# Performance work log

Hardware: AMD Instinct MI355X
Metric: run time of the kernel (lower is better)

## Reference

```python
import jax, jax.numpy as jnp
import numpy as np

N_NODES = 100000
N_EDGES = 1200000
D = 64          # node_feat_size
G_FEAT = 128    # graph_feat_size
N_GRAPHS = 256
N_TASKS = 1


def setup_inputs() -> dict:
    key = jax.random.key(0)
    ks = jax.random.split(key, 12)
    node_feats = jax.random.normal(ks[0], (N_NODES, D), dtype=jnp.float32)
    edge_feats = jax.random.normal(ks[1], (N_EDGES, 8), dtype=jnp.float32)
    src = jax.random.randint(ks[2], (N_EDGES,), 0, N_NODES, dtype=jnp.int64 if jax.config.read('jax_enable_x64') else jnp.int32)
    dst = jax.random.randint(ks[3], (N_EDGES,), 0, N_NODES, dtype=src.dtype)
    graph_ids = jnp.sort(jax.random.randint(ks[4], (N_NODES,), 0, N_GRAPHS, dtype=src.dtype))
    s = 1.0 / np.sqrt(D)
    W_gcn = jax.random.uniform(ks[5], (D, D), minval=-s, maxval=s, dtype=jnp.float32)
    b_gcn = jnp.zeros((D,), jnp.float32)
    W_res = jax.random.uniform(ks[6], (D, D), minval=-s, maxval=s, dtype=jnp.float32)
    b_res = jnp.zeros((D,), jnp.float32)
    W_in = jax.random.uniform(ks[7], (D, D), minval=-s, maxval=s, dtype=jnp.float32)
    b_in = jnp.zeros((D,), jnp.float32)
    W_out = jax.random.uniform(ks[8], (D, G_FEAT), minval=-s, maxval=s, dtype=jnp.float32)
    b_out = jnp.zeros((G_FEAT,), jnp.float32)
    sp = 1.0 / np.sqrt(G_FEAT)
    W_pred = jax.random.uniform(ks[9], (G_FEAT, N_TASKS), minval=-sp, maxval=sp, dtype=jnp.float32)
    b_pred = jnp.zeros((N_TASKS,), jnp.float32)
    return dict(node_feats=node_feats, edge_feats=edge_feats, src=src, dst=dst,
                graph_ids=graph_ids, W_gcn=W_gcn, b_gcn=b_gcn, W_res=W_res, b_res=b_res,
                W_in=W_in, b_in=b_in, W_out=W_out, b_out=b_out, W_pred=W_pred, b_pred=b_pred)


def reference(node_feats, edge_feats, src, dst, graph_ids,
              W_gcn, b_gcn, W_res, b_res, W_in, b_in, W_out, b_out, W_pred, b_pred):
    # --- GCNLayer (GraphConv norm='none', activation=relu, residual=True) ---
    # message passing: copy src features, sum at dst (no normalization)
    agg = jax.ops.segment_sum(node_feats[src], dst, num_segments=N_NODES)  # [N, D]
    h = jax.nn.relu(agg @ W_gcn + b_gcn)                                   # graph_conv output
    h = h + jax.nn.relu(node_feats @ W_res + b_res)                        # residual branch
    # --- MLPNodeReadout (mode='sum') ---
    h = jax.nn.relu(h @ W_in + b_in)      # [N, D]
    h = h @ W_out + b_out                 # [N, G_FEAT]
    g_feats = jax.ops.segment_sum(h, graph_ids, num_segments=N_GRAPHS)  # [G, G_FEAT]
    # --- predict ---
    out = (g_feats @ W_pred + b_pred).reshape(-1)  # [G * n_tasks]
    return out
```

## Files before the change

### kernel.cpp

```cpp
#include <hip/hip_runtime.h>

typedef __attribute__((ext_vector_type(8))) __bf16 bf16x8;
typedef __attribute__((ext_vector_type(4))) float f32x4;

union Frag { unsigned short u[8]; bf16x8 b; };

__device__ __forceinline__ unsigned short rne_bf16(float x) {
    unsigned int u = __float_as_uint(x);
    return (unsigned short)((u + 0x7fffu + ((u >> 16) & 1u)) >> 16);
}
__device__ __forceinline__ float bf16_to_f(unsigned short h) {
    return __uint_as_float(((unsigned int)h) << 16);
}

#define MFMA16 __builtin_amdgcn_mfma_f32_16x16x32_bf16
#define SBSH 10
#define SBN 1024
#define SBCAP 13056
#define BINCHUNK 4096
#define NWFRAG (3 * 2 * 2 * 4 * 64 * 8)

__global__ __launch_bounds__(256) void prepbinA_kernel(
    const float* __restrict__ nf, const int* __restrict__ src,
    const int* __restrict__ dst,
    const float* __restrict__ Wg, const float* __restrict__ Wr,
    const float* __restrict__ Wi, const float* __restrict__ Wo,
    const float* __restrict__ bo, const float* __restrict__ Wp,
    const float* __restrict__ bp,
    unsigned short* __restrict__ nfb, unsigned short* __restrict__ wfrag,
    float* __restrict__ wfold, float* __restrict__ c0, float* __restrict__ out,
    int* __restrict__ gcursor, int* __restrict__ binned,
    int nBin, int nE, int nbS, int out_size, int nNodes) {
    __shared__ int lhist[128], lbase[128], lofs[128];
    __shared__ int wtot;
    __shared__ int sortedV[BINCHUNK];
    __shared__ int sortedA[BINCHUNK];
    const int t = threadIdx.x;
    if ((int)blockIdx.x < nBin) {
        const int e0 = blockIdx.x * BINCHUNK;
        const int e1 = min(e0 + BINCHUNK, nE);
        const int cnt = e1 - e0;
        if (t < 128) lhist[t] = 0;
        __syncthreads();
        int myr[16];
        #pragma unroll
        for (int u = 0; u < 16; ++u) {
            int e = e0 + t + u * 256;
            if (e < e1) myr[u] = atomicAdd(&lhist[dst[e] >> SBSH], 1);
        }
        __syncthreads();
        int x = 0;
        if (t < 128) {
            x = lhist[t];
            #pragma unroll
            for (int s = 1; s < 64; s <<= 1) {
                int v = __shfl_up(x, s, 64);
                if ((t & 63) >= s) x += v;
            }
            if (t == 63) wtot = x;
        }
        __syncthreads();
        if (t < 128) {
            lofs[t] = x + ((t >= 64) ? wtot : 0);
            if (t < nbS) {
                int c = lhist[t];
                lbase[t] = c ? atomicAdd(&gcursor[t], c) : 0;
            }
        }
        __syncthreads();
        #pragma unroll
        for (int u = 0; u < 16; ++u) {
            int e = e0 + t + u * 256;
            if (e < e1) {
                int d = dst[e];
                int sb = d >> SBSH;
                int r = myr[u];
                int p = (lofs[sb] - lhist[sb]) + r;
                sortedV[p] = (src[e] << SBSH) | (d & (SBN - 1));
                int gp = lbase[sb] + r;
                sortedA[p] = (gp < SBCAP) ? (sb * SBCAP + gp) : -1;
            }
        }
        __syncthreads();
        for (int i = t; i < cnt; i += 256) {
            int ga = sortedA[i];
            if (ga >= 0) binned[ga] = sortedV[i];
        }
        return;
    }
    const int tp = ((int)blockIdx.x - nBin) * 256 + t;
    const int nth = ((int)gridDim.x - nBin) * 256;
    const float4* nf4 = (const float4*)nf;
    ushort4* nfb4 = (ushort4*)nfb;
    const int nQ = nNodes * 16;
    for (int i = tp; i < nQ; i += nth) {
        float4 v = nf4[i];
        ushort4 o;
        o.x = rne_bf16(v.x); o.y = rne_bf16(v.y);
        o.z = rne_bf16(v.z); o.w = rne_bf16(v.w);
        nfb4[i] = o;
    }
    const float* Ws[3] = {Wg, Wr, Wi};
    for (int idx = tp; idx < NWFRAG; idx += nth) {
        int j = idx & 7, lane = (idx >> 3) & 63, nt = (idx >> 9) & 3;
        int kt = (idx >> 11) & 1, part = (idx >> 12) & 1, mat = idx >> 13;
        int k = kt * 32 + ((lane >> 4) << 3) + j;
        int n = nt * 16 + (lane & 15);
        float w = Ws[mat][k * 64 + n];
        unsigned short hi = rne_bf16(w);
        wfrag[idx] = (part == 0) ? hi : rne_bf16(w - bf16_to_f(hi));
    }
    if (tp < 64) {
        float s = 0.f;
        for (int j = 0; j < 128; ++j) s += Wo[tp * 128 + j] * Wp[j];
        wfold[tp] = s;
    }
    if (tp == 0) {
        float s = 0.f;
        for (int j = 0; j < 128; ++j) s += bo[j] * Wp[j];
        c0[0] = s;
    }
    if (tp < out_size) out[tp] = bp[0];
}

__global__ __launch_bounds__(1024) void segB_kernel(
    int* __restrict__ binned, const int* __restrict__ gcursor,
    int2* __restrict__ nodeTab, int nNodes) {
    __shared__ int eL[SBCAP];
    __shared__ int deg[SBN], sc[SBN];
    __shared__ int wsum[16];
    const int b = blockIdx.x, t = threadIdx.x;
    const int cnt = min(gcursor[b], SBCAP);
    const int bb = b * SBCAP;
    deg[t] = 0;
    __syncthreads();
    int myr[13];
    #pragma unroll
    for (int u = 0; u < 13; ++u) {
        int i = t + u * 1024;
        if (i < cnt) {
            int p = binned[bb + i];
            eL[i] = p;
            myr[u] = atomicAdd(&deg[p & (SBN - 1)], 1);
        }
    }
    __syncthreads();
    const int lane = t & 63, w = t >> 6;
    int d = deg[t];
    int x = d;
    #pragma unroll
    for (int s = 1; s < 64; s <<= 1) {
        int v = __shfl_up(x, s, 64);
        if (lane >= s) x += v;
    }
    if (lane == 63) wsum[w] = x;
    __syncthreads();
    if (t < 16) {
        int y = wsum[t];
        #pragma unroll
        for (int s = 1; s < 16; s <<= 1) {
            int v = __shfl_up(y, s, 64);
            if (t >= s) y += v;
        }
        wsum[t] = y;
    }
    __syncthreads();
    {
        int incl = x + (w ? wsum[w - 1] : 0);
        int excl = incl - d;
        sc[t] = excl;
        int node = b * SBN + t;
        if (node < nNodes) nodeTab[node] = make_int2(bb + excl, d);
    }
    __syncthreads();
    #pragma unroll
    for (int u = 0; u < 13; ++u) {
        int i = t + u * 1024;
        if (i < cnt) {
            int p = eL[i];
            int pos = sc[p & (SBN - 1)] + myr[u];
            binned[bb + pos] = p >> SBSH;
        }
    }
}

__global__ __launch_bounds__(256) void gather_kernel(
    const unsigned short* __restrict__ nfb, const int2* __restrict__ nodeTab,
    const int* __restrict__ srcs, unsigned short* __restrict__ aggb, int nNodes) {
    int wid = blockIdx.x * 4 + (threadIdx.x >> 6);
    if (wid >= nNodes) return;
    int lane = threadIdx.x & 63;
    int half = lane >> 5;
    int cp = lane & 31;
    int2 sd = nodeTab[wid];
    int base = sd.x, d = sd.y;
    const ushort2* nfb2 = (const ushort2*)nfb;
    float ax = 0.f, ay = 0.f;
    if (d > 0 && d <= 64) {
        int myidx = srcs[base + min(lane, d - 1)];
        int dh = (d - half + 1) >> 1;
        for (int jb = 0; jb < dh; jb += 8) {
            int sA[8];
            #pragma unroll
            for (int u = 0; u < 8; ++u) {
                int e = 2 * (jb + u) + half;
                sA[u] = __shfl(myidx, (e < d) ? e : (d - 1), 64);
            }
            ushort2 v[8];
            #pragma unroll
            for (int u = 0; u < 8; ++u)
                v[u] = nfb2[(long)sA[u] * 32 + cp];
            #pragma unroll
            for (int u = 0; u < 8; ++u)
                if (jb + u < dh) { ax += bf16_to_f(v[u].x); ay += bf16_to_f(v[u].y); }
        }
    } else if (d > 64) {
        int k = half;
        for (; k + 8 <= d; k += 8) {
            int s0 = srcs[base + k],     s1 = srcs[base + k + 2];
            int s2 = srcs[base + k + 4], s3 = srcs[base + k + 6];
            ushort2 v0 = nfb2[(long)s0 * 32 + cp];
            ushort2 v1 = nfb2[(long)s1 * 32 + cp];
            ushort2 v2 = nfb2[(long)s2 * 32 + cp];
            ushort2 v3 = nfb2[(long)s3 * 32 + cp];
            ax += (bf16_to_f(v0.x) + bf16_to_f(v1.x)) + (bf16_to_f(v2.x) + bf16_to_f(v3.x));
            ay += (bf16_to_f(v0.y) + bf16_to_f(v1.y)) + (bf16_to_f(v2.y) + bf16_to_f(v3.y));
        }
        for (; k < d; k += 2) {
            int s = srcs[base + k];
            ushort2 v = nfb2[(long)s * 32 + cp];
            ax += bf16_to_f(v.x); ay += bf16_to_f(v.y);
        }
    }
    ax += __shfl_xor(ax, 32, 64);
    ay += __shfl_xor(ay, 32, 64);
    if (half == 0) {
        ushort2 o; o.x = rne_bf16(ax); o.y = rne_bf16(ay);
        ((ushort2*)aggb)[(long)wid * 32 + cp] = o;
    }
}

__global__ __launch_bounds__(256) void mlp_kernel(
    const unsigned short* __restrict__ aggb, const unsigned short* __restrict__ nfb,
    const int* __restrict__ gids, const unsigned short* __restrict__ wfrag,
    const float* __restrict__ bg, const float* __restrict__ br,
    const float* __restrict__ bi, const float* __restrict__ wfold,
    const float* __restrict__ c0p, float* __restrict__ out, int nTiles) {
    __shared__ float hs_all[4][32 * 68];
    const int wave = threadIdx.x >> 6, lane = threadIdx.x & 63;
    const int wid = blockIdx.x * 4 + wave;
    if (wid >= nTiles) return;
    float* hs = hs_all[wave];
    const int base = wid * 32;
    const int mrow = lane & 15, quad = lane >> 4;

    Frag aA[2][2], aN[2][2];
    #pragma unroll
    for (int rt = 0; rt < 2; ++rt) {
        const unsigned short* rowA = aggb + (long)(base + rt * 16 + mrow) * 64;
        const unsigned short* rowN = nfb  + (long)(base + rt * 16 + mrow) * 64;
        #pragma unroll
        for (int kt = 0; kt < 2; ++kt) {
            aA[rt][kt].b = *(const bf16x8*)(rowA + kt * 32 + quad * 8);
            aN[rt][kt].b = *(const bf16x8*)(rowN + kt * 32 + quad * 8);
        }
    }
    const unsigned short* wl0 = wfrag + lane * 8;
    auto WF = [&](int mat, int part, int kt, int nt) -> bf16x8 {
        return *(const bf16x8*)(wl0 + (size_t)((((mat * 2 + part) * 2 + kt) * 4 + nt) * 64) * 8);
    };
    f32x4 accA[2][4], accR[2][4];
    #pragma unroll
    for (int rt = 0; rt < 2; ++rt)
        #pragma unroll
        for (int nt = 0; nt < 4; ++nt) {
            accA[rt][nt] = (f32x4){0.f, 0.f, 0.f, 0.f};
            accR[rt][nt] = (f32x4){0.f, 0.f, 0.f, 0.f};
        }
    #pragma unroll
    for (int nt = 0; nt < 4; ++nt)
        #pragma unroll
        for (int kt = 0; kt < 2; ++kt) {
            bf16x8 gh = WF(0, 0, kt, nt), gl = WF(0, 1, kt, nt);
            bf16x8 rh = WF(1, 0, kt, nt), rl = WF(1, 1, kt, nt);
            #pragma unroll
            for (int rt = 0; rt < 2; ++rt) {
                accA[rt][nt] = MFMA16(aA[rt][kt].b, gh, accA[rt][nt], 0, 0, 0);
                accA[rt][nt] = MFMA16(aA[rt][kt].b, gl, accA[rt][nt], 0, 0, 0);
                accR[rt][nt] = MFMA16(aN[rt][kt].b, rh, accR[rt][nt], 0, 0, 0);
                accR[rt][nt] = MFMA16(aN[rt][kt].b, rl, accR[rt][nt], 0, 0, 0);
            }
        }
    #pragma unroll
    for (int nt = 0; nt < 4; ++nt) {
        float bgv = bg[nt * 16 + mrow], brv = br[nt * 16 + mrow];
        #pragma unroll
        for (int rt = 0; rt < 2; ++rt)
            #pragma unroll
            for (int r = 0; r < 4; ++r) {
                float h = fmaxf(accA[rt][nt][r] + bgv, 0.f)
                        + fmaxf(accR[rt][nt][r] + brv, 0.f);
                hs[(rt * 16 + quad * 4 + r) * 68 + nt * 16 + mrow] = h;
            }
    }
    __builtin_amdgcn_wave_barrier();
    Frag aH[2][2];
    #pragma unroll
    for (int rt = 0; rt < 2; ++rt)
        #pragma unroll
        for (int kt = 0; kt < 2; ++kt) {
            const float* hp = hs + (rt * 16 + mrow) * 68 + kt * 32 + quad * 8;
            float4 v0 = *(const float4*)hp;
            float4 v1 = *(const float4*)(hp + 4);
            aH[rt][kt].u[0] = rne_bf16(v0.x); aH[rt][kt].u[1] = rne_bf16(v0.y);
            aH[rt][kt].u[2] = rne_bf16(v0.z); aH[rt][kt].u[3] = rne_bf16(v0.w);
            aH[rt][kt].u[4] = rne_bf16(v1.x); aH[rt][kt].u[5] = rne_bf16(v1.y);
            aH[rt][kt].u[6] = rne_bf16(v1.z); aH[rt][kt].u[7] = rne_bf16(v1.w);
        }
    f32x4 accH[2][4];
    #pragma unroll
    for (int rt = 0; rt < 2; ++rt)
        #pragma unroll
        for (int nt = 0; nt < 4; ++nt)
            accH[rt][nt] = (f32x4){0.f, 0.f, 0.f, 0.f};
    #pragma unroll
    for (int nt = 0; nt < 4; ++nt)
        #pragma unroll
        for (int kt = 0; kt < 2; ++kt) {
            bf16x8 ih = WF(2, 0, kt, nt), il = WF(2, 1, kt, nt);
            #pragma unroll
            for (int rt = 0; rt < 2; ++rt) {
                accH[rt][nt] = MFMA16(aH[rt][kt].b, ih, accH[rt][nt], 0, 0, 0);
                accH[rt][nt] = MFMA16(aH[rt][kt].b, il, accH[rt][nt], 0, 0, 0);
            }
        }
    float p[2][4];
    #pragma unroll
    for (int rt = 0; rt < 2; ++rt)
        #pragma unroll
        for (int r = 0; r < 4; ++r) p[rt][r] = 0.f;
    #pragma unroll
    for (int nt = 0; nt < 4; ++nt) {
        float biv = bi[nt * 16 + mrow], wfv = wfold[nt * 16 + mrow];
        #pragma unroll
        for (int rt = 0; rt < 2; ++rt)
            #pragma unroll
            for (int r = 0; r < 4; ++r)
                p[rt][r] += fmaxf(accH[rt][nt][r] + biv, 0.f) * wfv;
    }
    #pragma unroll
    for (int m = 1; m <= 8; m <<= 1)
        #pragma unroll
        for (int rt = 0; rt < 2; ++rt)
            #pragma unroll
            for (int r = 0; r < 4; ++r)
                p[rt][r] += __shfl_xor(p[rt][r], m, 64);
    const float c0 = c0p[0];
    #pragma unroll
    for (int rt = 0; rt < 2; ++rt)
        #pragma unroll
        for (int r = 0; r < 4; ++r) p[rt][r] += c0;
    int gself = gids[base + (lane & 31)];
    int g0 = __shfl(gself, 0, 64);
    if (__all(gself == g0)) {
        float pv = 0.f;
        if (mrow == 0) {
            #pragma unroll
            for (int rt = 0; rt < 2; ++rt)
                #pragma unroll
                for (int r = 0; r < 4; ++r) pv += p[rt][r];
        }
        pv += __shfl_xor(pv, 16, 64);
        pv += __shfl_xor(pv, 32, 64);
        if (lane == 0) atomicAdd(out + g0, pv);
    } else if (mrow == 0) {
        #pragma unroll
        for (int rt = 0; rt < 2; ++rt)
            #pragma unroll
            for (int r = 0; r < 4; ++r)
                atomicAdd(out + gids[base + rt * 16 + quad * 4 + r], p[rt][r]);
    }
}

extern "C" void kernel_launch(void* const* d_in, const int* in_sizes, int n_in,
                              void* d_out, int out_size, void* d_ws, size_t ws_size,
                              hipStream_t stream) {
    const float* node_feats = (const float*)d_in[0];
    const int* src  = (const int*)d_in[2];
    const int* dst  = (const int*)d_in[3];
    const int* gids = (const int*)d_in[4];
    const float* Wg = (const float*)d_in[5];
    const float* bg = (const float*)d_in[6];
    const float* Wr = (const float*)d_in[7];
    const float* br = (const float*)d_in[8];
    const float* Wi = (const float*)d_in[9];
    const float* bi = (const float*)d_in[10];
    const float* Wo = (const float*)d_in[11];
    const float* bo = (const float*)d_in[12];
    const float* Wp = (const float*)d_in[13];
    const float* bp = (const float*)d_in[14];
    float* out = (float*)d_out;

    const int nNodes = in_sizes[0] / 64;
    const int nE = in_sizes[2];
    const int nbS = (nNodes + SBN - 1) / SBN;
    const int nBin = (nE + BINCHUNK - 1) / BINCHUNK;
    const int nTiles = (nNodes + 31) / 32;

    int* gcursor = (int*)d_ws;
    int* binned  = gcursor + 128;
    int2* nodeTab = (int2*)(binned + (size_t)nbS * SBCAP);
    unsigned short* nfb  = (unsigned short*)(nodeTab + nNodes);
    unsigned short* aggb = nfb + (size_t)nNodes * 64;
    unsigned short* wfrag = aggb + (size_t)nNodes * 64;
    float* wfold = (float*)(wfrag + NWFRAG);
    float* c0 = wfold + 64;

    hipMemsetAsync(gcursor, 0, 128 * sizeof(int), stream);

    prepbinA_kernel<<<nBin + 512, 256, 0, stream>>>(
        node_feats, src, dst, Wg, Wr, Wi, Wo, bo, Wp, bp,
        nfb, wfrag, wfold, c0, out, gcursor, binned,
        nBin, nE, nbS, out_size, nNodes);

    segB_kernel<<<nbS, 1024, 0, stream>>>(binned, gcursor, nodeTab, nNodes);

    gather_kernel<<<(nNodes + 3) / 4, 256, 0, stream>>>(nfb, nodeTab, binned, aggb, nNodes);

    mlp_kernel<<<(nTiles + 3) / 4, 256, 0, stream>>>(aggb, nfb, gids, wfrag,
        bg, br, bi, wfold, c0, out, nTiles);
}
```

Baseline: 209.7 us.

## Fuse neighbor gather into MLP kernel via per-wave shared-memory staging

Merges the gather and MLP kernels so each wave aggregates its own 32-node tile, one node at a time, writes the bf16 aggregates into its shared-memory tile buffer, and then runs the MFMA MLP on them. This drops one kernel launch and the global write and re-read of the aggregate array. In exchange, each wave now processes its 32 gathers serially, so there are about 32x fewer waves doing gather work and less memory-level parallelism to hide the random-access latency.

```diff
diff --git a/kernel.cpp b/kernel.cpp
--- a/kernel.cpp
+++ b/kernel.cpp
@@ -184,81 +184,85 @@
     }
 }
 
-__global__ __launch_bounds__(256) void gather_kernel(
+__global__ __launch_bounds__(256) void gmlp_kernel(
     const unsigned short* __restrict__ nfb, const int2* __restrict__ nodeTab,
-    const int* __restrict__ srcs, unsigned short* __restrict__ aggb, int nNodes) {
-    int wid = blockIdx.x * 4 + (threadIdx.x >> 6);
-    if (wid >= nNodes) return;
-    int lane = threadIdx.x & 63;
-    int half = lane >> 5;
-    int cp = lane & 31;
-    int2 sd = nodeTab[wid];
-    int base = sd.x, d = sd.y;
-    const ushort2* nfb2 = (const ushort2*)nfb;
-    float ax = 0.f, ay = 0.f;
-    if (d > 0 && d <= 64) {
-        int myidx = srcs[base + min(lane, d - 1)];
-        int dh = (d - half + 1) >> 1;
-        for (int jb = 0; jb < dh; jb += 8) {
-            int sA[8];
-            #pragma unroll
-            for (int u = 0; u < 8; ++u) {
-                int e = 2 * (jb + u) + half;
-                sA[u] = __shfl(myidx, (e < d) ? e : (d - 1), 64);
-            }
-            ushort2 v[8];
-            #pragma unroll
-            for (int u = 0; u < 8; ++u)
-                v[u] = nfb2[(long)sA[u] * 32 + cp];
-            #pragma unroll
-            for (int u = 0; u < 8; ++u)
-                if (jb + u < dh) { ax += bf16_to_f(v[u].x); ay += bf16_to_f(v[u].y); }
-        }
-    } else if (d > 64) {
-        int k = half;
-        for (; k + 8 <= d; k += 8) {
-            int s0 = srcs[base + k],     s1 = srcs[base + k + 2];
-            int s2 = srcs[base + k + 4], s3 = srcs[base + k + 6];
-            ushort2 v0 = nfb2[(long)s0 * 32 + cp];
-            ushort2 v1 = nfb2[(long)s1 * 32 + cp];
-            ushort2 v2 = nfb2[(long)s2 * 32 + cp];
-            ushort2 v3 = nfb2[(long)s3 * 32 + cp];
-            ax += (bf16_to_f(v0.x) + bf16_to_f(v1.x)) + (bf16_to_f(v2.x) + bf16_to_f(v3.x));
-            ay += (bf16_to_f(v0.y) + bf16_to_f(v1.y)) + (bf16_to_f(v2.y) + bf16_to_f(v3.y));
-        }
-        for (; k < d; k += 2) {
-            int s = srcs[base + k];
-            ushort2 v = nfb2[(long)s * 32 + cp];
-            ax += bf16_to_f(v.x); ay += bf16_to_f(v.y);
-        }
-    }
-    ax += __shfl_xor(ax, 32, 64);
-    ay += __shfl_xor(ay, 32, 64);
-    if (half == 0) {
-        ushort2 o; o.x = rne_bf16(ax); o.y = rne_bf16(ay);
-        ((ushort2*)aggb)[(long)wid * 32 + cp] = o;
-    }
-}
-
-__global__ __launch_bounds__(256) void mlp_kernel(
-    const unsigned short* __restrict__ aggb, const unsigned short* __restrict__ nfb,
-    const int* __restrict__ gids, const unsigned short* __restrict__ wfrag,
+    const int* __restrict__ srcs, const int* __restrict__ gids,
+    const unsigned short* __restrict__ wfrag,
     const float* __restrict__ bg, const float* __restrict__ br,
     const float* __restrict__ bi, const float* __restrict__ wfold,
-    const float* __restrict__ c0p, float* __restrict__ out, int nTiles) {
+    const float* __restrict__ c0p, float* __restrict__ out,
+    int nTiles, int nNodes) {
     __shared__ float hs_all[4][32 * 68];
     const int wave = threadIdx.x >> 6, lane = threadIdx.x & 63;
     const int wid = blockIdx.x * 4 + wave;
     if (wid >= nTiles) return;
     float* hs = hs_all[wave];
+    unsigned short* ag = (unsigned short*)hs;
     const int base = wid * 32;
+    const int half = lane >> 5, cp = lane & 31;
+    const ushort2* nfb2 = (const ushort2*)nfb;
+
+    int sdx = 0, sdy = 0;
+    if (lane < 32 && base + lane < nNodes) {
+        int2 sd = nodeTab[base + lane];
+        sdx = sd.x; sdy = sd.y;
+    }
+    for (int r = 0; r < 32; ++r) {
+        const int rbase = __shfl(sdx, r, 64);
+        const int d     = __shfl(sdy, r, 64);
+        float ax = 0.f, ay = 0.f;
+        if (d > 0 && d <= 64) {
+            int myidx = srcs[rbase + min(lane, d - 1)];
+            int dh = (d - half + 1) >> 1;
+            for (int jb = 0; jb < dh; jb += 8) {
+                int sA[8];
+                #pragma unroll
+                for (int u = 0; u < 8; ++u) {
+                    int e = 2 * (jb + u) + half;
+                    sA[u] = __shfl(myidx, (e < d) ? e : (d - 1), 64);
+                }
+                ushort2 v[8];
+                #pragma unroll
+                for (int u = 0; u < 8; ++u)
+                    v[u] = nfb2[(long)sA[u] * 32 + cp];
+                #pragma unroll
+                for (int u = 0; u < 8; ++u)
+                    if (jb + u < dh) { ax += bf16_to_f(v[u].x); ay += bf16_to_f(v[u].y); }
+            }
+        } else if (d > 64) {
+            int k = half;
+            for (; k + 8 <= d; k += 8) {
+                int s0 = srcs[rbase + k],     s1 = srcs[rbase + k + 2];
+                int s2 = srcs[rbase + k + 4], s3 = srcs[rbase + k + 6];
+                ushort2 v0 = nfb2[(long)s0 * 32 + cp];
+                ushort2 v1 = nfb2[(long)s1 * 32 + cp];
+                ushort2 v2 = nfb2[(long)s2 * 32 + cp];
+                ushort2 v3 = nfb2[(long)s3 * 32 + cp];
+                ax += (bf16_to_f(v0.x) + bf16_to_f(v1.x)) + (bf16_to_f(v2.x) + bf16_to_f(v3.x));
+                ay += (bf16_to_f(v0.y) + bf16_to_f(v1.y)) + (bf16_to_f(v2.y) + bf16_to_f(v3.y));
+            }
+            for (; k < d; k += 2) {
+                int s = srcs[rbase + k];
+                ushort2 v = nfb2[(long)s * 32 + cp];
+                ax += bf16_to_f(v.x); ay += bf16_to_f(v.y);
+            }
+        }
+        ax += __shfl_xor(ax, 32, 64);
+        ay += __shfl_xor(ay, 32, 64);
+        if (half == 0) {
+            ushort2 o; o.x = rne_bf16(ax); o.y = rne_bf16(ay);
+            *(ushort2*)(ag + r * 136 + 2 * cp) = o;
+        }
+    }
+    __builtin_amdgcn_wave_barrier();
+    asm volatile("" ::: "memory");
+
     const int mrow = lane & 15, quad = lane >> 4;
-
     Frag aA[2][2], aN[2][2];
     #pragma unroll
     for (int rt = 0; rt < 2; ++rt) {
-        const unsigned short* rowA = aggb + (long)(base + rt * 16 + mrow) * 64;
-        const unsigned short* rowN = nfb  + (long)(base + rt * 16 + mrow) * 64;
+        const unsigned short* rowA = ag + (rt * 16 + mrow) * 136;
+        const unsigned short* rowN = nfb + (long)(base + rt * 16 + mrow) * 64;
         #pragma unroll
         for (int kt = 0; kt < 2; ++kt) {
             aA[rt][kt].b = *(const bf16x8*)(rowA + kt * 32 + quad * 8);
@@ -291,6 +295,7 @@
                 accR[rt][nt] = MFMA16(aN[rt][kt].b, rl, accR[rt][nt], 0, 0, 0);
             }
         }
+    asm volatile("" ::: "memory");
     #pragma unroll
     for (int nt = 0; nt < 4; ++nt) {
         float bgv = bg[nt * 16 + mrow], brv = br[nt * 16 + mrow];
@@ -425,8 +430,6 @@
 
     segB_kernel<<<nbS, 1024, 0, stream>>>(binned, gcursor, nodeTab, nNodes);
 
-    gather_kernel<<<(nNodes + 3) / 4, 256, 0, stream>>>(nfb, nodeTab, binned, aggb, nNodes);
-
-    mlp_kernel<<<(nTiles + 3) / 4, 256, 0, stream>>>(aggb, nfb, gids, wfrag,
-        bg, br, bi, wfold, c0, out, nTiles);
-}
+    gmlp_kernel<<<(nTiles + 3) / 4, 256, 0, stream>>>(nfb, nodeTab, binned, gids,
+        wfrag, bg, br, bi, wfold, c0, out, nTiles, nNodes);
+}
```

After: 250.6 us. +19.5%, slower.

## Halve super-bin size and move bf16 prep work into segment-sort kernel

Applied to the files above, without the earlier changes.

Shrinks destination super-bins from 1024 to 512 nodes, so the second-pass sort runs on 196 blocks instead of 98 and fills more CUs. The bf16 conversion of node features and the weight-fragment prep move out of the binning kernel and run as extra blocks of the segment kernel, leaving the binning launch to do only edge binning. The binning histogram and scan are widened to 256 bins. Smaller per-bin capacity (7168) raises the risk of silently dropping edges if a bin overflows.

```diff
diff --git a/kernel.cpp b/kernel.cpp
--- a/kernel.cpp
+++ b/kernel.cpp
@@ -14,82 +14,153 @@
 }
 
 #define MFMA16 __builtin_amdgcn_mfma_f32_16x16x32_bf16
-#define SBSH 10
-#define SBN 1024
-#define SBCAP 13056
+#define SBSH 9
+#define SBN 512
+#define SBCAP 7168
 #define BINCHUNK 4096
 #define NWFRAG (3 * 2 * 2 * 4 * 64 * 8)
 
-__global__ __launch_bounds__(256) void prepbinA_kernel(
-    const float* __restrict__ nf, const int* __restrict__ src,
-    const int* __restrict__ dst,
+__global__ __launch_bounds__(256) void bin_kernel(
+    const int* __restrict__ src, const int* __restrict__ dst,
+    int* __restrict__ gcursor, int* __restrict__ binned,
+    int nE, int nbS) {
+    __shared__ int lhist[256], lbase[256], lofs[256];
+    __shared__ int wsum[4];
+    __shared__ int sortedV[BINCHUNK];
+    __shared__ int sortedA[BINCHUNK];
+    const int t = threadIdx.x;
+    const int e0 = blockIdx.x * BINCHUNK;
+    const int e1 = min(e0 + BINCHUNK, nE);
+    const int cnt = e1 - e0;
+    lhist[t] = 0;
+    __syncthreads();
+    int myr[16];
+    #pragma unroll
+    for (int u = 0; u < 16; ++u) {
+        int e = e0 + t + u * 256;
+        if (e < e1) myr[u] = atomicAdd(&lhist[dst[e] >> SBSH], 1);
+    }
+    __syncthreads();
+    const int lane = t & 63, w = t >> 6;
+    int x = lhist[t];
+    #pragma unroll
+    for (int s = 1; s < 64; s <<= 1) {
+        int v = __shfl_up(x, s, 64);
+        if (lane >= s) x += v;
+    }
+    if (lane == 63) wsum[w] = x;
+    __syncthreads();
+    if (t < 4) {
+        int y = wsum[t];
+        #pragma unroll
+        for (int s = 1; s < 4; s <<= 1) {
+            int v = __shfl_up(y, s, 64);
+            if (t >= s) y += v;
+        }
+        wsum[t] = y;
+    }
+    __syncthreads();
+    lofs[t] = x + (w ? wsum[w - 1] : 0);
+    if (t < nbS) {
+        int c = lhist[t];
+        lbase[t] = c ? atomicAdd(&gcursor[t], c) : 0;
+    }
+    __syncthreads();
+    #pragma unroll
+    for (int u = 0; u < 16; ++u) {
+        int e = e0 + t + u * 256;
+        if (e < e1) {
+            int d = dst[e];
+            int sb = d >> SBSH;
+            int r = myr[u];
+            int p = (lofs[sb] - lhist[sb]) + r;
+            sortedV[p] = (src[e] << SBSH) | (d & (SBN - 1));
+            int gp = lbase[sb] + r;
+            sortedA[p] = (gp < SBCAP) ? (sb * SBCAP + gp) : -1;
+        }
+    }
+    __syncthreads();
+    for (int i = t; i < cnt; i += 256) {
+        int ga = sortedA[i];
+        if (ga >= 0) binned[ga] = sortedV[i];
+    }
+}
+
+__global__ __launch_bounds__(1024) void segB_kernel(
+    int* __restrict__ binned, const int* __restrict__ gcursor,
+    int2* __restrict__ nodeTab,
+    const float* __restrict__ nf,
     const float* __restrict__ Wg, const float* __restrict__ Wr,
     const float* __restrict__ Wi, const float* __restrict__ Wo,
     const float* __restrict__ bo, const float* __restrict__ Wp,
     const float* __restrict__ bp,
     unsigned short* __restrict__ nfb, unsigned short* __restrict__ wfrag,
     float* __restrict__ wfold, float* __restrict__ c0, float* __restrict__ out,
-    int* __restrict__ gcursor, int* __restrict__ binned,
-    int nBin, int nE, int nbS, int out_size, int nNodes) {
-    __shared__ int lhist[128], lbase[128], lofs[128];
-    __shared__ int wtot;
-    __shared__ int sortedV[BINCHUNK];
-    __shared__ int sortedA[BINCHUNK];
-    const int t = threadIdx.x;
-    if ((int)blockIdx.x < nBin) {
-        const int e0 = blockIdx.x * BINCHUNK;
-        const int e1 = min(e0 + BINCHUNK, nE);
-        const int cnt = e1 - e0;
-        if (t < 128) lhist[t] = 0;
+    int nbS, int out_size, int nNodes) {
+    __shared__ int eL[SBCAP];
+    __shared__ int deg[SBN], sc[SBN];
+    __shared__ int wsum[8];
+    const int b = blockIdx.x, t = threadIdx.x;
+    if (b < nbS) {
+        const int cnt = min(gcursor[b], SBCAP);
+        const int bb = b * SBCAP;
+        if (t < SBN) deg[t] = 0;
         __syncthreads();
-        int myr[16];
-        #pragma unroll
-        for (int u = 0; u < 16; ++u) {
-            int e = e0 + t + u * 256;
-            if (e < e1) myr[u] = atomicAdd(&lhist[dst[e] >> SBSH], 1);
+        int myr[7];
+        #pragma unroll
+        for (int u = 0; u < 7; ++u) {
+            int i = t + u * 1024;
+            if (i < cnt) {
+                int p = binned[bb + i];
+                eL[i] = p;
+                myr[u] = atomicAdd(&deg[p & (SBN - 1)], 1);
+            }
         }
         __syncthreads();
-        int x = 0;
-        if (t < 128) {
-            x = lhist[t];
+        const int lane = t & 63, w = t >> 6;
+        if (t < SBN) {
+            int d = deg[t];
+            int x = d;
             #pragma unroll
             for (int s = 1; s < 64; s <<= 1) {
                 int v = __shfl_up(x, s, 64);
-                if ((t & 63) >= s) x += v;
-            }
-            if (t == 63) wtot = x;
+                if (lane >= s) x += v;
+            }
+            if (lane == 63) wsum[w] = x;
+            __syncthreads();
+            if (t < 8) {
+                int y = wsum[t];
+                #pragma unroll
+                for (int s = 1; s < 8; s <<= 1) {
+                    int v = __shfl_up(y, s, 64);
+                    if (t >= s) y += v;
+                }
+                wsum[t] = y;
+            }
+            __syncthreads();
+            int incl = x + (w ? wsum[w - 1] : 0);
+            int excl = incl - d;
+            sc[t] = excl;
+            int node = b * SBN + t;
+            if (node < nNodes) nodeTab[node] = make_int2(bb + excl, d);
+        } else {
+            __syncthreads();
+            __syncthreads();
         }
         __syncthreads();
-        if (t < 128) {
-            lofs[t] = x + ((t >= 64) ? wtot : 0);
-            if (t < nbS) {
-                int c = lhist[t];
-                lbase[t] = c ? atomicAdd(&gcursor[t], c) : 0;
-            }
-        }
-        __syncthreads();
-        #pragma unroll
-        for (int u = 0; u < 16; ++u) {
-            int e = e0 + t + u * 256;
-            if (e < e1) {
-                int d = dst[e];
-                int sb = d >> SBSH;
-                int r = myr[u];
-                int p = (lofs[sb] - lhist[sb]) + r;
-                sortedV[p] = (src[e] << SBSH) | (d & (SBN - 1));
-                int gp = lbase[sb] + r;
-                sortedA[p] = (gp < SBCAP) ? (sb * SBCAP + gp) : -1;
-            }
-        }
-        __syncthreads();
-        for (int i = t; i < cnt; i += 256) {
-            int ga = sortedA[i];
-            if (ga >= 0) binned[ga] = sortedV[i];
+        #pragma unroll
+        for (int u = 0; u < 7; ++u) {
+            int i = t + u * 1024;
+            if (i < cnt) {
+                int p = eL[i];
+                int pos = sc[p & (SBN - 1)] + myr[u];
+                binned[bb + pos] = p >> SBSH;
+            }
         }
         return;
     }
-    const int tp = ((int)blockIdx.x - nBin) * 256 + t;
-    const int nth = ((int)gridDim.x - nBin) * 256;
+    const int tp = ((int)blockIdx.x - nbS) * 1024 + t;
+    const int nth = ((int)gridDim.x - nbS) * 1024;
     const float4* nf4 = (const float4*)nf;
     ushort4* nfb4 = (ushort4*)nfb;
     const int nQ = nNodes * 16;
@@ -106,9 +177,9 @@
         int kt = (idx >> 11) & 1, part = (idx >> 12) & 1, mat = idx >> 13;
         int k = kt * 32 + ((lane >> 4) << 3) + j;
         int n = nt * 16 + (lane & 15);
-        float w = Ws[mat][k * 64 + n];
-        unsigned short hi = rne_bf16(w);
-        wfrag[idx] = (part == 0) ? hi : rne_bf16(w - bf16_to_f(hi));
+        float ww = Ws[mat][k * 64 + n];
+        unsigned short hi = rne_bf16(ww);
+        wfrag[idx] = (part == 0) ? hi : rne_bf16(ww - bf16_to_f(hi));
     }
     if (tp < 64) {
         float s = 0.f;
@@ -121,67 +192,6 @@
         c0[0] = s;
     }
     if (tp < out_size) out[tp] = bp[0];
-}
-
-__global__ __launch_bounds__(1024) void segB_kernel(
-    int* __restrict__ binned, const int* __restrict__ gcursor,
-    int2* __restrict__ nodeTab, int nNodes) {
-    __shared__ int eL[SBCAP];
-    __shared__ int deg[SBN], sc[SBN];
-    __shared__ int wsum[16];
-    const int b = blockIdx.x, t = threadIdx.x;
-    const int cnt = min(gcursor[b], SBCAP);
-    const int bb = b * SBCAP;
-    deg[t] = 0;
-    __syncthreads();
-    int myr[13];
-    #pragma unroll
-    for (int u = 0; u < 13; ++u) {
-        int i = t + u * 1024;
-        if (i < cnt) {
-            int p = binned[bb + i];
-            eL[i] = p;
-            myr[u] = atomicAdd(&deg[p & (SBN - 1)], 1);
-        }
-    }
-    __syncthreads();
-    const int lane = t & 63, w = t >> 6;
-    int d = deg[t];
-    int x = d;
-    #pragma unroll
-    for (int s = 1; s < 64; s <<= 1) {
-        int v = __shfl_up(x, s, 64);
-        if (lane >= s) x += v;
-    }
-    if (lane == 63) wsum[w] = x;
-    __syncthreads();
-    if (t < 16) {
-        int y = wsum[t];
-        #pragma unroll
-        for (int s = 1; s < 16; s <<= 1) {
-            int v = __shfl_up(y, s, 64);
-            if (t >= s) y += v;
-        }
-        wsum[t] = y;
-    }
-    __syncthreads();
-    {
-        int incl = x + (w ? wsum[w - 1] : 0);
-        int excl = incl - d;
-        sc[t] = excl;
-        int node = b * SBN + t;
-        if (node < nNodes) nodeTab[node] = make_int2(bb + excl, d);
-    }
-    __syncthreads();
-    #pragma unroll
-    for (int u = 0; u < 13; ++u) {
-        int i = t + u * 1024;
-        if (i < cnt) {
-            int p = eL[i];
-            int pos = sc[p & (SBN - 1)] + myr[u];
-            binned[bb + pos] = p >> SBSH;
-        }
-    }
 }
 
 __global__ __launch_bounds__(256) void gather_kernel(
@@ -408,7 +418,7 @@
     const int nTiles = (nNodes + 31) / 32;
 
     int* gcursor = (int*)d_ws;
-    int* binned  = gcursor + 128;
+    int* binned  = gcursor + 256;
     int2* nodeTab = (int2*)(binned + (size_t)nbS * SBCAP);
     unsigned short* nfb  = (unsigned short*)(nodeTab + nNodes);
     unsigned short* aggb = nfb + (size_t)nNodes * 64;
@@ -416,14 +426,13 @@
     float* wfold = (float*)(wfrag + NWFRAG);
     float* c0 = wfold + 64;
 
-    hipMemsetAsync(gcursor, 0, 128 * sizeof(int), stream);
-
-    prepbinA_kernel<<<nBin + 512, 256, 0, stream>>>(
-        node_feats, src, dst, Wg, Wr, Wi, Wo, bo, Wp, bp,
-        nfb, wfrag, wfold, c0, out, gcursor, binned,
-        nBin, nE, nbS, out_size, nNodes);
-
-    segB_kernel<<<nbS, 1024, 0, stream>>>(binned, gcursor, nodeTab, nNodes);
+    hipMemsetAsync(gcursor, 0, 256 * sizeof(int), stream);
+
+    bin_kernel<<<nBin, 256, 0, stream>>>(src, dst, gcursor, binned, nE, nbS);
+
+    segB_kernel<<<nbS + 256, 1024, 0, stream>>>(binned, gcursor, nodeTab,
+        node_feats, Wg, Wr, Wi, Wo, bo, Wp, bp,
+        nfb, wfrag, wfold, c0, out, nbS, out_size, nNodes);
 
     gather_kernel<<<(nNodes + 3) / 4, 256, 0, stream>>>(nfb, nodeTab, binned, aggb, nNodes);
 
```

New measurement: 210.2 us. About the same (+0.2%).
